# Performance work log

Hardware: AMD Instinct MI355X
Metric: run time of the kernel (lower is better)

Reference implementation:

```python
import jax, jax.numpy as jnp
import numpy as np

S, N, IN = 4096, 32, 4
H, IF, SF, OUT = 64, 8, 4, 2
N_PAIRS = N * (N - 1)


def setup_inputs() -> dict:
    key = jax.random.key(0)
    ks = jax.random.split(key, 12)
    f = jax.random.normal
    return {
        "inputs": f(ks[0], (S, N, IN), jnp.float32),
        "L1W": f(ks[1], (H, IN), jnp.float32) * 0.1,
        "L1b": f(ks[2], (H,), jnp.float32) * 0.1,
        "L2W": f(ks[3], (H, H), jnp.float32) * 0.1,
        "L2b": f(ks[4], (H,), jnp.float32) * 0.1,
        "I1W": f(ks[5], (H, H), jnp.float32) * 0.1,
        "I2W": f(ks[6], (IF, H), jnp.float32) * 0.1,
        "I3": f(ks[7], (N_PAIRS, OUT, IF // OUT), jnp.float32) * 0.01,
        "S1W": f(ks[8], (SF, IN), jnp.float32) * 0.1,
        "S1b": f(ks[9], (SF,), jnp.float32) * 0.1,
        "S2W": f(ks[10], (N, OUT, SF // OUT), jnp.float32) * 0.01,
        "S2b": jnp.zeros((N, OUT), jnp.float32),
    }


def reference(inputs, L1W, L1b, L2W, L2b, I1W, I2W, I3, S1W, S1b, S2W, S2b):
    seq_len, n_obj = inputs.shape[:2]
    out_size = S2b.shape[1]

    # shared encoders (torch Linear: x @ W.T + b)
    h = jax.nn.relu(inputs @ L1W.T + L1b)
    h = jax.nn.relu(h @ L2W.T + L2b)          # [S, N, H]
    hs = jax.nn.relu(inputs @ S1W.T + S1b)    # [S, N, SF]

    # all pairwise differences Xi - Xj -> edge MLP (no biases)
    diff = h[:, :, None, :] - h[:, None, :, :]      # [S, N, N, H]
    pair = jnp.tanh(diff @ I1W.T)                   # [S, N, N, H]
    pair = jnp.tanh(pair @ I2W.T)                   # [S, N, N, IF]
    k_int = pair.shape[-1] // out_size
    pair = pair.reshape(seq_len, n_obj, n_obj, out_size, k_int)

    # scatter per-pair weights I3 into dense [N, N, OUT, k] using the
    # row-major Table ordering (i, j != i); diagonal stays zero, which
    # matches the original since diag pairwise features are exactly 0.
    ii, jj = np.nonzero(~np.eye(n_obj, dtype=bool))
    I3d = jnp.zeros((n_obj, n_obj, out_size, k_int), I3.dtype).at[ii, jj].set(I3)

    interaction = jnp.einsum('sijdk,ijdk->sid', pair, I3d)  # [S, N, OUT]

    k_self = hs.shape[-1] // out_size
    hs = hs.reshape(seq_len, n_obj, out_size, k_self)
    self_term = jnp.einsum('sidk,idk->sid', hs, S2W) + S2b  # [S, N, OUT]

    return interaction + self_term
```

## Files before the change

### kernel.cpp

```cpp
#include <hip/hip_runtime.h>
#include <math.h>

#define SEQ   4096
#define NOBJ  32
#define IN_F  4
#define HID   64
#define IFEAT 8
#define NPAIR_HALF 496
#define NTILE 31

#define TWO_LOG2E 2.8853900817779268f
#define GP_CLAMP  10.0f

#if __has_builtin(__builtin_amdgcn_exp2f)
  #define EXP2F(x) __builtin_amdgcn_exp2f(x)
#else
  #define EXP2F(x) exp2f(x)
#endif

typedef _Float16 h2    __attribute__((ext_vector_type(2)));
typedef _Float16 f16x8 __attribute__((ext_vector_type(8)));
typedef short    s16x8 __attribute__((ext_vector_type(8)));
typedef float    f32x4 __attribute__((ext_vector_type(4)));

__device__ __forceinline__ h2 pack2(float a, float b) {
  return __builtin_bit_cast(h2, __builtin_amdgcn_cvt_pkrtz(a, b));
}
__device__ __forceinline__ unsigned pbits(h2 v) { return __builtin_bit_cast(unsigned, v); }

__device__ __forceinline__ f16x8 pack8(float4 a, float4 b) {
  int4 v;
  v.x = (int)pbits(pack2(a.x, a.y));
  v.y = (int)pbits(pack2(a.z, a.w));
  v.z = (int)pbits(pack2(b.x, b.y));
  v.w = (int)pbits(pack2(b.z, b.w));
  return __builtin_bit_cast(f16x8, v);
}

__device__ __forceinline__ f16x8 rcp8nr(f16x8 x) {
  const s16x8 magic = (short)0x7799;
  f16x8 r = __builtin_bit_cast(f16x8, (s16x8)(magic - __builtin_bit_cast(s16x8, x)));
  const f16x8 two = (_Float16)2.0f;
  const f16x8 nx = -x;
#if __has_builtin(__builtin_elementwise_fma)
  r = r * __builtin_elementwise_fma(nx, r, two);
  r = r * __builtin_elementwise_fma(nx, r, two);
#else
  r = r * (nx * r + two);
  r = r * (nx * r + two);
#endif
  return r;
}

__device__ __forceinline__ float dot2h(h2 a, h2 b, float c) {
#if __has_builtin(__builtin_amdgcn_fdot2)
  return __builtin_amdgcn_fdot2(a, b, c, false);
#else
  float r = c;
  r = fmaf((float)a.x, (float)b.x, r);
  r = fmaf((float)a.y, (float)b.y, r);
  return r;
#endif
}

__device__ __forceinline__ float xor8_f32(float v) {
#if __has_builtin(__builtin_amdgcn_mov_dpp)
  return __builtin_bit_cast(float,
      __builtin_amdgcn_mov_dpp(__builtin_bit_cast(int, v), 0x128, 0xF, 0xF, true));
#else
  return __shfl_xor(v, 8, 16);
#endif
}

__device__ __forceinline__ int pair_cum(int i) { return (i * (63 - i)) >> 1; }

__device__ __forceinline__ void pair_decode(int q, int& i, int& j) {
  int ii = (int)((63.0f - sqrtf(3969.0f - 8.0f * (float)q)) * 0.5f);
  if (ii > 0 && pair_cum(ii) > q) --ii;
  if (pair_cum(ii + 1) <= q)     ++ii;
  i = ii;
  j = ii + 1 + (q - pair_cum(ii));
}

__global__ __launch_bounds__(256, 4) void magnet_fused(
    const float* __restrict__ x,
    const float* __restrict__ L1W,
    const float* __restrict__ L1b,
    const float* __restrict__ L2W,
    const float* __restrict__ L2b,
    const float* __restrict__ I1W,
    const float* __restrict__ I2W,
    const float* __restrict__ I3,
    const float* __restrict__ S1W,
    const float* __restrict__ S1b,
    const float* __restrict__ S2W,
    const float* __restrict__ S2b,
    float* __restrict__ out)
{
  __shared__ __align__(16) float smem[15544];
  unsigned*       sEd0 = (unsigned*)(smem + 9920);
  unsigned*       wB   = (unsigned*)(smem + 14528);
  float*          sW   = smem + 15040;
  unsigned*       ptab32 = (unsigned*)(smem + 15048);
  float*          swpart = smem + 9920;

  const int t  = threadIdx.x;
  const int s0 = blockIdx.x * 4;

  if (t < 64) {
    const int f = t >> 3, seg = t & 7;
    const float4 a = *(const float4*)(I2W + f * HID + seg * 8);
    const float4 b = *(const float4*)(I2W + f * HID + seg * 8 + 4);
    swpart[t] = ((a.x + a.y) + (a.z + a.w)) + ((b.x + b.y) + (b.z + b.w));
  }
  #pragma unroll
  for (int idx = t; idx < 512; idx += 256) {
    const int n = idx >> 5, k2 = idx & 31;
    wB[idx] = (n < IFEAT)
      ? pbits(pack2(I2W[n * HID + 2 * k2], I2W[n * HID + 2 * k2 + 1])) : 0u;
  }
  #pragma unroll
  for (int q = t; q < NPAIR_HALF; q += 256) {
    int i, j; pair_decode(q, i, j);
    ptab32[q] = ((unsigned)(i * 36) << 16) | (unsigned)(j * 36);
  }

  {
    const int n = t & 31, gI = t >> 5, kb = gI * 8;
    float4 xv[4];
    #pragma unroll
    for (int ss = 0; ss < 4; ++ss)
      xv[ss] = *(const float4*)(x + (s0 + ss) * 128 + n * 4);
    float a[4][8];
    #pragma unroll
    for (int r = 0; r < 8; ++r) {
      const int k = kb + r;
      const float4 w = *(const float4*)(L1W + k * 4);
      const float bias = L1b[k];
      #pragma unroll
      for (int ss = 0; ss < 4; ++ss) {
        float v = bias;
        v = fmaf(xv[ss].x, w.x, v); v = fmaf(xv[ss].y, w.y, v);
        v = fmaf(xv[ss].z, w.z, v); v = fmaf(xv[ss].w, w.w, v);
        a[ss][r] = fmaxf(v, 0.0f);
      }
    }
    #pragma unroll
    for (int ss = 0; ss < 4; ++ss) {
      unsigned* sAtp = (unsigned*)(smem + ss * 1152);
      int4 pk;
      pk.x = (int)pbits(pack2(a[ss][0], a[ss][1]));
      pk.y = (int)pbits(pack2(a[ss][2], a[ss][3]));
      pk.z = (int)pbits(pack2(a[ss][4], a[ss][5]));
      pk.w = (int)pbits(pack2(a[ss][6], a[ss][7]));
      *(int4*)(sAtp + n * 36 + gI * 4) = pk;
    }
  }
  __syncthreads();

  if (t < IFEAT) {
    float a = 0.0f;
    #pragma unroll
    for (int c = 0; c < 8; ++c) a += swpart[t * 8 + c];
    sW[t] = a;
  }

  const int lane = t & 63;
  const int wv   = t >> 6;
  const int qd   = lane >> 4;
  const int ln   = lane & 15;

  {
    const int m = 16 * wv + ln;
    const float* wr = L2W + m * HID;
    const f16x8 A0 = pack8(*(const float4*)(wr + 8 * qd),
                           *(const float4*)(wr + 8 * qd + 4));
    const f16x8 A1 = pack8(*(const float4*)(wr + 32 + 8 * qd),
                           *(const float4*)(wr + 32 + 8 * qd + 4));
    const float4 bias = *(const float4*)(L2b + 16 * wv + 4 * qd);
    #pragma unroll
    for (int ss = 0; ss < 4; ++ss) {
      const unsigned* sAtp = (const unsigned*)(smem + ss * 1152);
      unsigned* sBtp = (unsigned*)(smem + 4608 + ss * 1152);
      #pragma unroll
      for (int nt = 0; nt < 2; ++nt) {
        const int n = nt * 16 + ln;
        const f16x8 B0 = __builtin_bit_cast(f16x8, *(const int4*)(sAtp + n * 36 + 4 * qd));
        const f16x8 B1 = __builtin_bit_cast(f16x8, *(const int4*)(sAtp + n * 36 + 16 + 4 * qd));
        f32x4 c; c[0] = bias.x; c[1] = bias.y; c[2] = bias.z; c[3] = bias.w;
        c = __builtin_amdgcn_mfma_f32_16x16x32_f16(A0, B0, c, 0, 0, 0);
        c = __builtin_amdgcn_mfma_f32_16x16x32_f16(A1, B1, c, 0, 0, 0);
        sBtp[n * 36 + 8 * wv + 2 * qd]     = pbits(pack2(fmaxf(c[0], 0.f), fmaxf(c[1], 0.f)));
        sBtp[n * 36 + 8 * wv + 2 * qd + 1] = pbits(pack2(fmaxf(c[2], 0.f), fmaxf(c[3], 0.f)));
      }
    }
  }
  __syncthreads();

  {
    const int m = 16 * wv + ln;
    const float* wr = I1W + m * HID;
    float4 w0 = *(const float4*)(wr + 8 * qd);
    float4 w1 = *(const float4*)(wr + 8 * qd + 4);
    float4 w2 = *(const float4*)(wr + 32 + 8 * qd);
    float4 w3 = *(const float4*)(wr + 32 + 8 * qd + 4);
    const float T = TWO_LOG2E;
    w0.x *= T; w0.y *= T; w0.z *= T; w0.w *= T;
    w1.x *= T; w1.y *= T; w1.z *= T; w1.w *= T;
    w2.x *= T; w2.y *= T; w2.z *= T; w2.w *= T;
    w3.x *= T; w3.y *= T; w3.z *= T; w3.w *= T;
    const f16x8 A0 = pack8(w0, w1);
    const f16x8 A1 = pack8(w2, w3);
    #pragma unroll
    for (int ss = 0; ss < 4; ++ss) {
      const unsigned* sBtp = (const unsigned*)(smem + 4608 + ss * 1152);
      unsigned* sEd = sEd0 + ss * 1152;
      #pragma unroll
      for (int nt = 0; nt < 2; ++nt) {
        const int n = nt * 16 + ln;
        const f16x8 B0 = __builtin_bit_cast(f16x8, *(const int4*)(sBtp + n * 36 + 4 * qd));
        const f16x8 B1 = __builtin_bit_cast(f16x8, *(const int4*)(sBtp + n * 36 + 16 + 4 * qd));
        f32x4 c; c[0] = 0.f; c[1] = 0.f; c[2] = 0.f; c[3] = 0.f;
        c = __builtin_amdgcn_mfma_f32_16x16x32_f16(A0, B0, c, 0, 0, 0);
        c = __builtin_amdgcn_mfma_f32_16x16x32_f16(A1, B1, c, 0, 0, 0);
        float e[4];
        #pragma unroll
        for (int r = 0; r < 4; ++r) {
          float gp = fminf(fmaxf(c[r], -GP_CLAMP), GP_CLAMP);
          e[r] = EXP2F(gp);
        }
        sEd[n * 36 + 8 * wv + 2 * qd]     = pbits(pack2(e[0], e[1]));
        sEd[n * 36 + 8 * wv + 2 * qd + 1] = pbits(pack2(e[2], e[3]));
      }
    }
  }
  __syncthreads();

  {
    const f16x8 B0 = __builtin_bit_cast(f16x8, *(const int4*)(wB + ln * 32 + 4 * qd));
    const f16x8 B1 = __builtin_bit_cast(f16x8, *(const int4*)(wB + ln * 32 + 16 + 4 * qd));
    const float WfT = sW[ln & 7] * TWO_LOG2E;
    const float n2T = -2.0f * TWO_LOG2E;
    const bool lo = (ln < IFEAT);
    const int col = ln & 7;

    for (int tile = wv; tile < NTILE; tile += 4) {
      const unsigned pij = ptab32[tile * 16 + ln];
      const int io = (int)(pij >> 16), jo = (int)(pij & 0xffffu);
      #pragma unroll
      for (int sp = 0; sp < 2; ++sp) {
        f32x4 c0, c1;
        #pragma unroll
        for (int half = 0; half < 2; ++half) {
          const unsigned* sEd = sEd0 + (2 * sp + half) * 1152;
          const f16x8 ei0 = __builtin_bit_cast(f16x8, *(const int4*)(sEd + io + 4 * qd));
          const f16x8 ei1 = __builtin_bit_cast(f16x8, *(const int4*)(sEd + io + 16 + 4 * qd));
          const f16x8 fj0 = __builtin_bit_cast(f16x8, *(const int4*)(sEd + jo + 4 * qd));
          const f16x8 fj1 = __builtin_bit_cast(f16x8, *(const int4*)(sEd + jo + 16 + 4 * qd));
          const f16x8 su0 = ei0 + fj0;
          const f16x8 su1 = ei1 + fj1;
          const f16x8 A0 = fj0 * rcp8nr(su0);
          const f16x8 A1 = fj1 * rcp8nr(su1);
          f32x4 c; c[0] = 0.f; c[1] = 0.f; c[2] = 0.f; c[3] = 0.f;
          c = __builtin_amdgcn_mfma_f32_16x16x32_f16(A0, B0, c, 0, 0, 0);
          c = __builtin_amdgcn_mfma_f32_16x16x32_f16(A1, B1, c, 0, 0, 0);
          if (half == 0) c0 = c; else c1 = c;
        }
        _Float16* svb = lo ? ((_Float16*)smem + (2 * sp) * 4960)
                           : ((_Float16*)smem + (2 * sp + 1) * 4960);
        #pragma unroll
        for (int r = 0; r < 4; ++r) {
          const float c1s = xor8_f32(c1[r]);
          const float m = lo ? c0[r] : c1s;
          const float arg = fmaf(n2T, m, WfT);
          const float e = EXP2F(arg);
          const float rr = __builtin_amdgcn_rcpf(e + 1.0f);
          const float v = fmaf(-2.0f, rr, 1.0f);
          svb[(tile * 16 + 4 * qd + r) * 10 + col] = (_Float16)v;
        }
      }
    }
  }
  __syncthreads();

  {
    const int ss = t >> 6, i = (t >> 1) & 31, d = t & 1;
    const _Float16* sv = (const _Float16*)smem + ss * 4960;
    const int Ci = pair_cum(i);
    float sum = 0.0f;
    #pragma unroll
    for (int m = 0; m < 31; ++m) {
      const bool up = (m >= i);
      const int q = up ? (Ci + m - i) : (pair_cum(m) + i - m - 1);
      const h2* vp = (const h2*)(sv + q * 10 + d * 4);
      const h2 va = vp[0], vb = vp[1];
      const float4 cf = *(const float4*)(I3 + (i * 31 + m) * 8 + d * 4);
      const h2 ca = pack2(cf.x, cf.y);
      const h2 cb = pack2(cf.z, cf.w);
      float dot = dot2h(va, ca, 0.0f);
      dot = dot2h(vb, cb, dot);
      const float sgn = up ? 1.0f : -1.0f;
      sum = fmaf(sgn, dot, sum);
    }

    float res = S2b[i * 2 + d] + sum;
    const float4 xv = *(const float4*)(x + (s0 + ss) * 128 + i * 4);
    #pragma unroll
    for (int k = 0; k < 2; ++k) {
      const int f = d * 2 + k;
      float hs = S1b[f];
      hs = fmaf(xv.x, S1W[f * 4 + 0], hs);
      hs = fmaf(xv.y, S1W[f * 4 + 1], hs);
      hs = fmaf(xv.z, S1W[f * 4 + 2], hs);
      hs = fmaf(xv.w, S1W[f * 4 + 3], hs);
      hs = fmaxf(hs, 0.0f);
      res = fmaf(hs, S2W[i * 4 + d * 2 + k], res);
    }
    out[(s0 + ss) * (NOBJ * 2) + i * 2 + d] = res;
  }
}

extern "C" void kernel_launch(void* const* d_in, const int* in_sizes, int n_in,
                              void* d_out, int out_size, void* d_ws, size_t ws_size,
                              hipStream_t stream) {
  const float* x   = (const float*)d_in[0];
  const float* L1W = (const float*)d_in[1];
  const float* L1b = (const float*)d_in[2];
  const float* L2W = (const float*)d_in[3];
  const float* L2b = (const float*)d_in[4];
  const float* I1W = (const float*)d_in[5];
  const float* I2W = (const float*)d_in[6];
  const float* I3  = (const float*)d_in[7];
  const float* S1W = (const float*)d_in[8];
  const float* S1b = (const float*)d_in[9];
  const float* S2W = (const float*)d_in[10];
  const float* S2b = (const float*)d_in[11];
  float* outp = (float*)d_out;

  magnet_fused<<<SEQ / 4, 256, 0, stream>>>(x, L1W, L1b, L2W, L2b, I1W, I2W, I3,
                                            S1W, S1b, S2W, S2b, outp);
}
```

Measured before the change: 109.6 us.

## Assign one sequence step per wavefront and drop block-wide barriers

The work split changes from four sequence steps shared across the whole block to one sequence step per wavefront. Each wave computes layer 1 straight into MFMA B-operand registers, runs the L2 and I1 GEMMs over all four M tiles, and handles all 31 pair tiles with one pair of MFMAs per tile. All but one __syncthreads are gone, I2W operands and its row sums are built in registers with shuffles, and the per-wave shared buffers shrink. The cost is that every wave now reloads and repacks the full L2W and I1W weights, which adds register pressure and redundant global loads.

After: 116.4 us. +6.2%, slower.

```diff
diff --git a/kernel.cpp b/kernel.cpp
--- a/kernel.cpp
+++ b/kernel.cpp
@@ -22,6 +22,7 @@
 typedef _Float16 f16x8 __attribute__((ext_vector_type(8)));
 typedef short    s16x8 __attribute__((ext_vector_type(8)));
 typedef float    f32x4 __attribute__((ext_vector_type(4)));
+typedef unsigned u32x2 __attribute__((ext_vector_type(2)));
 
 __device__ __forceinline__ h2 pack2(float a, float b) {
   return __builtin_bit_cast(h2, __builtin_amdgcn_cvt_pkrtz(a, b));
@@ -34,6 +35,15 @@
   v.y = (int)pbits(pack2(a.z, a.w));
   v.z = (int)pbits(pack2(b.x, b.y));
   v.w = (int)pbits(pack2(b.z, b.w));
+  return __builtin_bit_cast(f16x8, v);
+}
+
+__device__ __forceinline__ f16x8 pack8a(const float* a) {
+  int4 v;
+  v.x = (int)pbits(pack2(a[0], a[1]));
+  v.y = (int)pbits(pack2(a[2], a[3]));
+  v.z = (int)pbits(pack2(a[4], a[5]));
+  v.w = (int)pbits(pack2(a[6], a[7]));
   return __builtin_bit_cast(f16x8, v);
 }
 
@@ -97,214 +107,203 @@
     const float* __restrict__ S2b,
     float* __restrict__ out)
 {
-  __shared__ __align__(16) float smem[15544];
-  unsigned*       sEd0 = (unsigned*)(smem + 9920);
-  unsigned*       wB   = (unsigned*)(smem + 14528);
-  float*          sW   = smem + 15040;
-  unsigned*       ptab32 = (unsigned*)(smem + 15048);
-  float*          swpart = smem + 9920;
-
-  const int t  = threadIdx.x;
-  const int s0 = blockIdx.x * 4;
-
-  if (t < 64) {
-    const int f = t >> 3, seg = t & 7;
-    const float4 a = *(const float4*)(I2W + f * HID + seg * 8);
-    const float4 b = *(const float4*)(I2W + f * HID + seg * 8 + 4);
-    swpart[t] = ((a.x + a.y) + (a.z + a.w)) + ((b.x + b.y) + (b.z + b.w));
-  }
-  #pragma unroll
-  for (int idx = t; idx < 512; idx += 256) {
-    const int n = idx >> 5, k2 = idx & 31;
-    wB[idx] = (n < IFEAT)
-      ? pbits(pack2(I2W[n * HID + 2 * k2], I2W[n * HID + 2 * k2 + 1])) : 0u;
-  }
+  __shared__ __align__(16) float smem[13040];
+
+  const int t    = threadIdx.x;
+  const int lane = t & 63;
+  const int wv   = t >> 6;
+  const int s    = blockIdx.x * 4 + wv;
+  const int qd   = lane >> 4;
+  const int ln   = lane & 15;
+
+  float*    Awf = smem + wv * 1984;
+  unsigned* stg = (unsigned*)Awf;
+  _Float16* sv  = (_Float16*)Awf;
+  unsigned* E   = (unsigned*)(smem + 7936 + wv * 1152);
+  unsigned* ptab32 = (unsigned*)(smem + 12544);
+
   #pragma unroll
   for (int q = t; q < NPAIR_HALF; q += 256) {
     int i, j; pair_decode(q, i, j);
     ptab32[q] = ((unsigned)(i * 36) << 16) | (unsigned)(j * 36);
   }
 
-  {
-    const int n = t & 31, gI = t >> 5, kb = gI * 8;
-    float4 xv[4];
-    #pragma unroll
-    for (int ss = 0; ss < 4; ++ss)
-      xv[ss] = *(const float4*)(x + (s0 + ss) * 128 + n * 4);
-    float a[4][8];
+  float WfT;
+  {
+    const int f = lane >> 3, seg = lane & 7;
+    const float4 a = *(const float4*)(I2W + f * HID + seg * 8);
+    const float4 b = *(const float4*)(I2W + f * HID + seg * 8 + 4);
+    float p = ((a.x + a.y) + (a.z + a.w)) + ((b.x + b.y) + (b.z + b.w));
+    p += __shfl_xor(p, 1, 8);
+    p += __shfl_xor(p, 2, 8);
+    p += __shfl_xor(p, 4, 8);
+    WfT = __shfl(p, (ln & 7) * 8, 64) * TWO_LOG2E;
+  }
+
+  f16x8 B4a0, B4a1;
+  {
+    const int n8 = (ln < IFEAT) ? ln : 0;
+    const float* wr = I2W + n8 * HID;
+    const f16x8 b0 = pack8(*(const float4*)(wr + 8 * qd),
+                           *(const float4*)(wr + 8 * qd + 4));
+    const f16x8 b1 = pack8(*(const float4*)(wr + 32 + 8 * qd),
+                           *(const float4*)(wr + 32 + 8 * qd + 4));
+    const f16x8 z = (_Float16)0.0f;
+    B4a0 = (ln < IFEAT) ? b0 : z;
+    B4a1 = (ln < IFEAT) ? b1 : z;
+  }
+
+  f16x8 hLo0, hHi0, hLo1, hHi1;
+  {
+    const float4 x0 = *(const float4*)(x + s * 128 + ln * 4);
+    const float4 x1 = *(const float4*)(x + s * 128 + (16 + ln) * 4);
+    float aLo0[8], aHi0[8], aLo1[8], aHi1[8];
     #pragma unroll
     for (int r = 0; r < 8; ++r) {
-      const int k = kb + r;
-      const float4 w = *(const float4*)(L1W + k * 4);
-      const float bias = L1b[k];
-      #pragma unroll
-      for (int ss = 0; ss < 4; ++ss) {
-        float v = bias;
-        v = fmaf(xv[ss].x, w.x, v); v = fmaf(xv[ss].y, w.y, v);
-        v = fmaf(xv[ss].z, w.z, v); v = fmaf(xv[ss].w, w.w, v);
-        a[ss][r] = fmaxf(v, 0.0f);
-      }
-    }
-    #pragma unroll
-    for (int ss = 0; ss < 4; ++ss) {
-      unsigned* sAtp = (unsigned*)(smem + ss * 1152);
-      int4 pk;
-      pk.x = (int)pbits(pack2(a[ss][0], a[ss][1]));
-      pk.y = (int)pbits(pack2(a[ss][2], a[ss][3]));
-      pk.z = (int)pbits(pack2(a[ss][4], a[ss][5]));
-      pk.w = (int)pbits(pack2(a[ss][6], a[ss][7]));
-      *(int4*)(sAtp + n * 36 + gI * 4) = pk;
-    }
-  }
+      {
+        const int k = 8 * qd + r;
+        const float4 wk = *(const float4*)(L1W + k * 4);
+        const float bias = L1b[k];
+        float v0 = bias, v1 = bias;
+        v0 = fmaf(x0.x, wk.x, v0); v0 = fmaf(x0.y, wk.y, v0);
+        v0 = fmaf(x0.z, wk.z, v0); v0 = fmaf(x0.w, wk.w, v0);
+        v1 = fmaf(x1.x, wk.x, v1); v1 = fmaf(x1.y, wk.y, v1);
+        v1 = fmaf(x1.z, wk.z, v1); v1 = fmaf(x1.w, wk.w, v1);
+        aLo0[r] = fmaxf(v0, 0.0f); aLo1[r] = fmaxf(v1, 0.0f);
+      }
+      {
+        const int k = 32 + 8 * qd + r;
+        const float4 wk = *(const float4*)(L1W + k * 4);
+        const float bias = L1b[k];
+        float v0 = bias, v1 = bias;
+        v0 = fmaf(x0.x, wk.x, v0); v0 = fmaf(x0.y, wk.y, v0);
+        v0 = fmaf(x0.z, wk.z, v0); v0 = fmaf(x0.w, wk.w, v0);
+        v1 = fmaf(x1.x, wk.x, v1); v1 = fmaf(x1.y, wk.y, v1);
+        v1 = fmaf(x1.z, wk.z, v1); v1 = fmaf(x1.w, wk.w, v1);
+        aHi0[r] = fmaxf(v0, 0.0f); aHi1[r] = fmaxf(v1, 0.0f);
+      }
+    }
+    hLo0 = pack8a(aLo0); hHi0 = pack8a(aHi0);
+    hLo1 = pack8a(aLo1); hHi1 = pack8a(aHi1);
+  }
+
   __syncthreads();
 
-  if (t < IFEAT) {
-    float a = 0.0f;
-    #pragma unroll
-    for (int c = 0; c < 8; ++c) a += swpart[t * 8 + c];
-    sW[t] = a;
-  }
-
-  const int lane = t & 63;
-  const int wv   = t >> 6;
-  const int qd   = lane >> 4;
-  const int ln   = lane & 15;
-
-  {
-    const int m = 16 * wv + ln;
-    const float* wr = L2W + m * HID;
-    const f16x8 A0 = pack8(*(const float4*)(wr + 8 * qd),
-                           *(const float4*)(wr + 8 * qd + 4));
-    const f16x8 A1 = pack8(*(const float4*)(wr + 32 + 8 * qd),
-                           *(const float4*)(wr + 32 + 8 * qd + 4));
-    const float4 bias = *(const float4*)(L2b + 16 * wv + 4 * qd);
-    #pragma unroll
-    for (int ss = 0; ss < 4; ++ss) {
-      const unsigned* sAtp = (const unsigned*)(smem + ss * 1152);
-      unsigned* sBtp = (unsigned*)(smem + 4608 + ss * 1152);
+  {
+    #pragma unroll
+    for (int mt = 0; mt < 4; ++mt) {
+      const float* wr = L2W + (16 * mt + ln) * HID;
+      const f16x8 A0 = pack8(*(const float4*)(wr + 8 * qd),
+                             *(const float4*)(wr + 8 * qd + 4));
+      const f16x8 A1 = pack8(*(const float4*)(wr + 32 + 8 * qd),
+                             *(const float4*)(wr + 32 + 8 * qd + 4));
+      const float4 bias = *(const float4*)(L2b + 16 * mt + 4 * qd);
       #pragma unroll
       for (int nt = 0; nt < 2; ++nt) {
-        const int n = nt * 16 + ln;
-        const f16x8 B0 = __builtin_bit_cast(f16x8, *(const int4*)(sAtp + n * 36 + 4 * qd));
-        const f16x8 B1 = __builtin_bit_cast(f16x8, *(const int4*)(sAtp + n * 36 + 16 + 4 * qd));
         f32x4 c; c[0] = bias.x; c[1] = bias.y; c[2] = bias.z; c[3] = bias.w;
-        c = __builtin_amdgcn_mfma_f32_16x16x32_f16(A0, B0, c, 0, 0, 0);
-        c = __builtin_amdgcn_mfma_f32_16x16x32_f16(A1, B1, c, 0, 0, 0);
-        sBtp[n * 36 + 8 * wv + 2 * qd]     = pbits(pack2(fmaxf(c[0], 0.f), fmaxf(c[1], 0.f)));
-        sBtp[n * 36 + 8 * wv + 2 * qd + 1] = pbits(pack2(fmaxf(c[2], 0.f), fmaxf(c[3], 0.f)));
-      }
-    }
-  }
-  __syncthreads();
-
-  {
-    const int m = 16 * wv + ln;
-    const float* wr = I1W + m * HID;
-    float4 w0 = *(const float4*)(wr + 8 * qd);
-    float4 w1 = *(const float4*)(wr + 8 * qd + 4);
-    float4 w2 = *(const float4*)(wr + 32 + 8 * qd);
-    float4 w3 = *(const float4*)(wr + 32 + 8 * qd + 4);
+        c = __builtin_amdgcn_mfma_f32_16x16x32_f16(A0, nt ? hLo1 : hLo0, c, 0, 0, 0);
+        c = __builtin_amdgcn_mfma_f32_16x16x32_f16(A1, nt ? hHi1 : hHi0, c, 0, 0, 0);
+        u32x2 pr;
+        pr.x = pbits(pack2(fmaxf(c[0], 0.f), fmaxf(c[1], 0.f)));
+        pr.y = pbits(pack2(fmaxf(c[2], 0.f), fmaxf(c[3], 0.f)));
+        *(u32x2*)(stg + (nt * 16 + ln) * 36 + 8 * mt + 2 * qd) = pr;
+      }
+    }
+  }
+
+  {
+    const int n0 = ln, n1 = 16 + ln;
+    const f16x8 Bs00 = __builtin_bit_cast(f16x8, *(const int4*)(stg + n0 * 36 + 4 * qd));
+    const f16x8 Bs01 = __builtin_bit_cast(f16x8, *(const int4*)(stg + n0 * 36 + 16 + 4 * qd));
+    const f16x8 Bs10 = __builtin_bit_cast(f16x8, *(const int4*)(stg + n1 * 36 + 4 * qd));
+    const f16x8 Bs11 = __builtin_bit_cast(f16x8, *(const int4*)(stg + n1 * 36 + 16 + 4 * qd));
     const float T = TWO_LOG2E;
-    w0.x *= T; w0.y *= T; w0.z *= T; w0.w *= T;
-    w1.x *= T; w1.y *= T; w1.z *= T; w1.w *= T;
-    w2.x *= T; w2.y *= T; w2.z *= T; w2.w *= T;
-    w3.x *= T; w3.y *= T; w3.z *= T; w3.w *= T;
-    const f16x8 A0 = pack8(w0, w1);
-    const f16x8 A1 = pack8(w2, w3);
-    #pragma unroll
-    for (int ss = 0; ss < 4; ++ss) {
-      const unsigned* sBtp = (const unsigned*)(smem + 4608 + ss * 1152);
-      unsigned* sEd = sEd0 + ss * 1152;
+    #pragma unroll
+    for (int mt = 0; mt < 4; ++mt) {
+      const float* wr = I1W + (16 * mt + ln) * HID;
+      float4 w0 = *(const float4*)(wr + 8 * qd);
+      float4 w1 = *(const float4*)(wr + 8 * qd + 4);
+      float4 w2 = *(const float4*)(wr + 32 + 8 * qd);
+      float4 w3 = *(const float4*)(wr + 32 + 8 * qd + 4);
+      w0.x *= T; w0.y *= T; w0.z *= T; w0.w *= T;
+      w1.x *= T; w1.y *= T; w1.z *= T; w1.w *= T;
+      w2.x *= T; w2.y *= T; w2.z *= T; w2.w *= T;
+      w3.x *= T; w3.y *= T; w3.z *= T; w3.w *= T;
+      const f16x8 A0 = pack8(w0, w1);
+      const f16x8 A1 = pack8(w2, w3);
       #pragma unroll
       for (int nt = 0; nt < 2; ++nt) {
-        const int n = nt * 16 + ln;
-        const f16x8 B0 = __builtin_bit_cast(f16x8, *(const int4*)(sBtp + n * 36 + 4 * qd));
-        const f16x8 B1 = __builtin_bit_cast(f16x8, *(const int4*)(sBtp + n * 36 + 16 + 4 * qd));
         f32x4 c; c[0] = 0.f; c[1] = 0.f; c[2] = 0.f; c[3] = 0.f;
-        c = __builtin_amdgcn_mfma_f32_16x16x32_f16(A0, B0, c, 0, 0, 0);
-        c = __builtin_amdgcn_mfma_f32_16x16x32_f16(A1, B1, c, 0, 0, 0);
+        c = __builtin_amdgcn_mfma_f32_16x16x32_f16(A0, nt ? Bs10 : Bs00, c, 0, 0, 0);
+        c = __builtin_amdgcn_mfma_f32_16x16x32_f16(A1, nt ? Bs11 : Bs01, c, 0, 0, 0);
         float e[4];
         #pragma unroll
         for (int r = 0; r < 4; ++r) {
-          float gp = fminf(fmaxf(c[r], -GP_CLAMP), GP_CLAMP);
+          const float gp = fminf(fmaxf(c[r], -GP_CLAMP), GP_CLAMP);
           e[r] = EXP2F(gp);
         }
-        sEd[n * 36 + 8 * wv + 2 * qd]     = pbits(pack2(e[0], e[1]));
-        sEd[n * 36 + 8 * wv + 2 * qd + 1] = pbits(pack2(e[2], e[3]));
-      }
-    }
-  }
-  __syncthreads();
-
-  {
-    const f16x8 B0 = __builtin_bit_cast(f16x8, *(const int4*)(wB + ln * 32 + 4 * qd));
-    const f16x8 B1 = __builtin_bit_cast(f16x8, *(const int4*)(wB + ln * 32 + 16 + 4 * qd));
-    const float WfT = sW[ln & 7] * TWO_LOG2E;
+        u32x2 pr;
+        pr.x = pbits(pack2(e[0], e[1]));
+        pr.y = pbits(pack2(e[2], e[3]));
+        *(u32x2*)(E + (nt * 16 + ln) * 36 + 8 * mt + 2 * qd) = pr;
+      }
+    }
+  }
+
+  {
     const float n2T = -2.0f * TWO_LOG2E;
     const bool lo = (ln < IFEAT);
     const int col = ln & 7;
-
-    for (int tile = wv; tile < NTILE; tile += 4) {
+    const int rofs = lo ? 0 : 1;
+
+    #pragma unroll 2
+    for (int tile = 0; tile < NTILE; ++tile) {
       const unsigned pij = ptab32[tile * 16 + ln];
       const int io = (int)(pij >> 16), jo = (int)(pij & 0xffffu);
+      const f16x8 ei0 = __builtin_bit_cast(f16x8, *(const int4*)(E + io + 4 * qd));
+      const f16x8 ei1 = __builtin_bit_cast(f16x8, *(const int4*)(E + io + 16 + 4 * qd));
+      const f16x8 fj0 = __builtin_bit_cast(f16x8, *(const int4*)(E + jo + 4 * qd));
+      const f16x8 fj1 = __builtin_bit_cast(f16x8, *(const int4*)(E + jo + 16 + 4 * qd));
+      const f16x8 su0 = ei0 + fj0;
+      const f16x8 su1 = ei1 + fj1;
+      const f16x8 A0 = fj0 * rcp8nr(su0);
+      const f16x8 A1 = fj1 * rcp8nr(su1);
+      f32x4 c; c[0] = 0.f; c[1] = 0.f; c[2] = 0.f; c[3] = 0.f;
+      c = __builtin_amdgcn_mfma_f32_16x16x32_f16(A0, B4a0, c, 0, 0, 0);
+      c = __builtin_amdgcn_mfma_f32_16x16x32_f16(A1, B4a1, c, 0, 0, 0);
       #pragma unroll
-      for (int sp = 0; sp < 2; ++sp) {
-        f32x4 c0, c1;
-        #pragma unroll
-        for (int half = 0; half < 2; ++half) {
-          const unsigned* sEd = sEd0 + (2 * sp + half) * 1152;
-          const f16x8 ei0 = __builtin_bit_cast(f16x8, *(const int4*)(sEd + io + 4 * qd));
-          const f16x8 ei1 = __builtin_bit_cast(f16x8, *(const int4*)(sEd + io + 16 + 4 * qd));
-          const f16x8 fj0 = __builtin_bit_cast(f16x8, *(const int4*)(sEd + jo + 4 * qd));
-          const f16x8 fj1 = __builtin_bit_cast(f16x8, *(const int4*)(sEd + jo + 16 + 4 * qd));
-          const f16x8 su0 = ei0 + fj0;
-          const f16x8 su1 = ei1 + fj1;
-          const f16x8 A0 = fj0 * rcp8nr(su0);
-          const f16x8 A1 = fj1 * rcp8nr(su1);
-          f32x4 c; c[0] = 0.f; c[1] = 0.f; c[2] = 0.f; c[3] = 0.f;
-          c = __builtin_amdgcn_mfma_f32_16x16x32_f16(A0, B0, c, 0, 0, 0);
-          c = __builtin_amdgcn_mfma_f32_16x16x32_f16(A1, B1, c, 0, 0, 0);
-          if (half == 0) c0 = c; else c1 = c;
-        }
-        _Float16* svb = lo ? ((_Float16*)smem + (2 * sp) * 4960)
-                           : ((_Float16*)smem + (2 * sp + 1) * 4960);
-        #pragma unroll
-        for (int r = 0; r < 4; ++r) {
-          const float c1s = xor8_f32(c1[r]);
-          const float m = lo ? c0[r] : c1s;
-          const float arg = fmaf(n2T, m, WfT);
-          const float e = EXP2F(arg);
-          const float rr = __builtin_amdgcn_rcpf(e + 1.0f);
-          const float v = fmaf(-2.0f, rr, 1.0f);
-          svb[(tile * 16 + 4 * qd + r) * 10 + col] = (_Float16)v;
-        }
-      }
-    }
-  }
-  __syncthreads();
-
-  {
-    const int ss = t >> 6, i = (t >> 1) & 31, d = t & 1;
-    const _Float16* sv = (const _Float16*)smem + ss * 4960;
+      for (int rb = 0; rb < 4; rb += 2) {
+        const float cns = xor8_f32(c[rb + 1]);
+        const float m = lo ? c[rb] : cns;
+        const float arg = fmaf(n2T, m, WfT);
+        const float e = EXP2F(arg);
+        const float rr = __builtin_amdgcn_rcpf(e + 1.0f);
+        const float v = fmaf(-2.0f, rr, 1.0f);
+        sv[(tile * 16 + 4 * qd + rb + rofs) * 8 + col] = (_Float16)v;
+      }
+    }
+  }
+
+  {
+    const int i = lane >> 1, d = lane & 1;
     const int Ci = pair_cum(i);
     float sum = 0.0f;
     #pragma unroll
     for (int m = 0; m < 31; ++m) {
       const bool up = (m >= i);
       const int q = up ? (Ci + m - i) : (pair_cum(m) + i - m - 1);
-      const h2* vp = (const h2*)(sv + q * 10 + d * 4);
+      const h2* vp = (const h2*)(sv + q * 8 + d * 4);
       const h2 va = vp[0], vb = vp[1];
       const float4 cf = *(const float4*)(I3 + (i * 31 + m) * 8 + d * 4);
       const h2 ca = pack2(cf.x, cf.y);
       const h2 cb = pack2(cf.z, cf.w);
       float dot = dot2h(va, ca, 0.0f);
       dot = dot2h(vb, cb, dot);
-      const float sgn = up ? 1.0f : -1.0f;
-      sum = fmaf(sgn, dot, sum);
+      sum = fmaf(up ? 1.0f : -1.0f, dot, sum);
     }
 
     float res = S2b[i * 2 + d] + sum;
-    const float4 xv = *(const float4*)(x + (s0 + ss) * 128 + i * 4);
+    const float4 xv = *(const float4*)(x + s * 128 + i * 4);
     #pragma unroll
     for (int k = 0; k < 2; ++k) {
       const int f = d * 2 + k;
@@ -316,7 +315,7 @@
       hs = fmaxf(hs, 0.0f);
       res = fmaf(hs, S2W[i * 4 + d * 2 + k], res);
     }
-    out[(s0 + ss) * (NOBJ * 2) + i * 2 + d] = res;
+    out[s * (NOBJ * 2) + i * 2 + d] = res;
   }
 }
 
```
